# Optimization experiments

Measured on AMD Instinct MI355X. Metric: run time of the kernel, lower is better.

Reference implementation:

```python
import jax, jax.numpy as jnp
import numpy as np

B, CIN, COUT, KH, KW = 8, 64, 128, 3, 3
H = W = 64
STRIDE, PAD = 1, 1
G = 1  # deformable groups


def setup_inputs() -> dict:
    key = jax.random.key(0)
    k1, k2, k3 = jax.random.split(key, 3)
    rgb = jax.random.normal(k1, (B, CIN, H, W), dtype=jnp.float32)
    # torchvision layout: [B, 2*G*KH*KW, Ho, Wo], (dy, dx) pairs per kernel tap
    offsets = jax.random.normal(k2, (B, 2 * G * KH * KW, H, W), dtype=jnp.float32)
    # xavier_uniform for weight [COUT, CIN, KH, KW]
    fan_in, fan_out = CIN * KH * KW, COUT * KH * KW
    a = float(np.sqrt(6.0 / (fan_in + fan_out)))
    weight = jax.random.uniform(k3, (COUT, CIN, KH, KW), dtype=jnp.float32, minval=-a, maxval=a)
    bias = jnp.zeros((COUT,), dtype=jnp.float32)
    return {"rgb": rgb, "offsets": offsets, "weight": weight, "bias": bias}


def _deform_conv2d(rgb, offsets, weight, bias):
    b, cin, h, w = rgb.shape
    cout, _, kh, kw = weight.shape
    K = kh * kw
    ho = (h + 2 * PAD - kh) // STRIDE + 1
    wo = (w + 2 * PAD - kw) // STRIDE + 1
    cg = cin // G  # channels per deformable group

    off = offsets.reshape(b, G, K, 2, ho, wo)
    dy, dx = off[:, :, :, 0], off[:, :, :, 1]  # [b, G, K, ho, wo]

    ky, kx = jnp.meshgrid(jnp.arange(kh), jnp.arange(kw), indexing="ij")
    ky = ky.reshape(K).astype(jnp.float32)
    kx = kx.reshape(K).astype(jnp.float32)
    base_y = (jnp.arange(ho) * STRIDE - PAD).astype(jnp.float32)
    base_x = (jnp.arange(wo) * STRIDE - PAD).astype(jnp.float32)

    # sampling coordinates: p0 + kernel tap + learned offset -> [b, G, K, ho, wo]
    y = base_y[None, None, None, :, None] + ky[None, None, :, None, None] + dy
    x = base_x[None, None, None, None, :] + kx[None, None, :, None, None] + dx

    y0 = jnp.floor(y)
    x0 = jnp.floor(x)
    fy = y - y0
    fx = x - x0
    y0i = y0.astype(jnp.int32)
    x0i = x0.astype(jnp.int32)

    x_flat = rgb.reshape(b, G, cg, h * w)
    P = K * ho * wo

    def gather_corner(yc, xc, wgt):
        valid = (yc >= 0) & (yc < h) & (xc >= 0) & (xc < w)
        idx = jnp.clip(yc, 0, h - 1) * w + jnp.clip(xc, 0, w - 1)
        wgt = jnp.where(valid, wgt, 0.0).reshape(b, G, 1, P)
        vals = jnp.take_along_axis(x_flat, idx.reshape(b, G, 1, P), axis=3)
        return vals * wgt

    col = (
        gather_corner(y0i, x0i, (1 - fy) * (1 - fx))
        + gather_corner(y0i, x0i + 1, (1 - fy) * fx)
        + gather_corner(y0i + 1, x0i, fy * (1 - fx))
        + gather_corner(y0i + 1, x0i + 1, fy * fx)
    )  # [b, G, cg, K*ho*wo]

    col = col.reshape(b, cin * K, ho * wo)
    out = jnp.einsum("ok,bkp->bop", weight.reshape(cout, cin * K), col)
    return out.reshape(b, cout, ho, wo) + bias[None, :, None, None]


def reference(rgb, offsets, weight, bias):
    return _deform_conv2d(rgb, offsets, weight, bias)
```

## Files before the change

### kernel.cpp

```cpp
#include <hip/hip_runtime.h>

#define COUT_  128
#define KP     1024
#define CAPR   20
#define IMGC   (21 * 64)
#define IMGBUF (4 * IMGC)
#define COLU   36
#define COLBUF (64 * COLU)
#define WS_NEED (size_t)(COUT_ * KP * 2 + 8ull * 64 * 64 * 64 * 4)

#if __has_builtin(__builtin_amdgcn_fdot2_f32_bf16)
#define HAS_DOT2 1
#else
#define HAS_DOT2 0
#endif

typedef __attribute__((ext_vector_type(8))) __bf16 bf16x8;
typedef __attribute__((ext_vector_type(2))) __bf16 bf16x2;
typedef unsigned short u16x8 __attribute__((ext_vector_type(8)));
typedef __attribute__((ext_vector_type(4))) float f32x4;

__device__ __forceinline__ unsigned int f2bf(float f) {
    union { float f; unsigned int u; } c; c.f = f;
    unsigned int u = c.u;
    u += 0x7fffu + ((u >> 16) & 1u);
    return u >> 16;
}
__device__ __forceinline__ float bitsf(unsigned int u) {
    union { unsigned int u; float f; } c; c.u = u; return c.f;
}
__device__ __forceinline__ unsigned int pk2bf(float lo, float hi) {
    return f2bf(lo) | (f2bf(hi) << 16);
}
__device__ __forceinline__ bf16x2 mk_bf2(float lo, float hi) {
    unsigned int u = pk2bf(lo, hi);
    return __builtin_bit_cast(bf16x2, u);
}
__device__ __forceinline__ void gl_lds16(const unsigned int* g, unsigned int* l) {
    __builtin_amdgcn_global_load_lds(
        (const __attribute__((address_space(1))) unsigned int*)g,
        (__attribute__((address_space(3))) unsigned int*)l, 16, 0, 0);
}

__global__ void prep_weight(const float* __restrict__ w, unsigned short* __restrict__ wbf) {
    int idx = blockIdx.x * 256 + threadIdx.x;
    if (idx >= COUT_ * KP) return;
    int cout = idx >> 10, r = idx & 1023;
    int quad = r >> 6, j2 = r & 63;
    int k = j2 >> 2, j = j2 & 3;
    unsigned short v = 0;
    if (k < 9) {
        int cin = quad * 4 + j;
        v = (unsigned short)f2bf(w[(cout * 64 + cin) * 9 + k]);
    }
    wbf[idx] = v;
}

__global__ void prep_rgb(const float* __restrict__ rgb, unsigned int* __restrict__ rgbp) {
    int idx = blockIdx.x * 256 + threadIdx.x;
    float a = rgb[idx];
    float nb = ((idx & 63) == 63) ? 0.f : rgb[idx + 1];
    rgbp[idx] = f2bf(a) | (f2bf(nb) << 16);
}

template<bool PREP>
__launch_bounds__(256, 2)
__global__ void deform_mfma6(const float* __restrict__ rgb,
                             const unsigned int* __restrict__ rgbp,
                             const float* __restrict__ off,
                             const unsigned short* __restrict__ wbf,
                             const float* __restrict__ bias,
                             float* __restrict__ out) {
    __shared__ unsigned int S[2 * COLBUF + 2 * IMGBUF];
    __shared__ int sYmin, sYmax;
    unsigned int* imgU = S + 2 * COLBUF;

    const int t    = threadIdx.x;
    const int bid  = blockIdx.x;
    const int b    = bid & 7;
    const int ho   = bid >> 3;
    const int lane = t & 63;
    const int wv   = t >> 6;
    const int px   = lane;
    const int ln15 = lane & 15;
    const int q    = lane >> 4;

    const float* offb = off + b * (2 * 9 * 4096);

    {
        uint4* S4 = (uint4*)S;
        for (int i = t; i < (2 * COLBUF + 2 * IMGBUF) / 4; i += 256)
            S4[i] = make_uint4(0, 0, 0, 0);
    }
    if (t == 0) { sYmin = 64; sYmax = -1; }
    __syncthreads();

    float m_fy[3], m_fx[3]; int m_y0[3], m_x0[3];
    int lmin = 64, lmax = -1;
#pragma unroll
    for (int ti = 0; ti < 3; ti++) {
        const int kt = (ti < 2) ? (wv + ti * 4) : 8;
        const float dy = offb[((2 * kt)     * 64 + ho) * 64 + px];
        const float dx = offb[((2 * kt + 1) * 64 + ho) * 64 + px];
        const float y = (float)(ho - 1 + kt / 3) + dy;
        const float x = (float)(px - 1 + kt % 3) + dx;
        const float y0f = floorf(y), x0f = floorf(x);
        m_fy[ti] = y - y0f; m_fx[ti] = x - x0f;
        m_y0[ti] = (int)y0f; m_x0[ti] = (int)x0f;
        const int r0 = min(max(m_y0[ti], 0), 63), r1 = min(max(m_y0[ti] + 1, 0), 63);
        lmin = min(lmin, r0); lmax = max(lmax, r1);
    }
    atomicMin(&sYmin, lmin); atomicMax(&sYmax, lmax);
    __syncthreads();
    const int ymin  = sYmin;
    const int nrows = sYmax - ymin + 1;
    const int nr4   = min((nrows + 3) & ~3, CAPR);
    const int ymin2 = max(0, min(ymin, 64 - nr4));

    float4 sv[5];
    auto stage_dma = [&](int gg) {
        const unsigned int* gp = rgbp + ((unsigned)(b * 64 + gg * 4 + wv) * 64 + ymin2) * 64 + lane * 4;
        unsigned int* lp = imgU + (gg & 1) * IMGBUF + wv * IMGC;
        for (int r4 = 0; r4 < nr4; r4 += 4) gl_lds16(gp + r4 * 64, lp + r4 * 64);
    };
    auto stage_load = [&](int gg) {
        const float* gp = rgb + ((unsigned)(b * 64 + gg * 4 + wv) * 64 + ymin2 + (lane >> 4)) * 64 + (lane & 15) * 4;
        int n = 0;
        for (int r4 = 0; r4 < nr4; r4 += 4, n++) sv[n] = *(const float4*)(gp + r4 * 64);
    };
    auto stage_write = [&](int gg) {
        unsigned int* lp = imgU + (gg & 1) * IMGBUF + wv * IMGC + (lane >> 4) * 64 + (lane & 15) * 4;
        int n = 0;
        for (int r4 = 0; r4 < nr4; r4 += 4, n++) {
            const float4 v = sv[n];
            unsigned int b0 = f2bf(v.x), b1 = f2bf(v.y), b2 = f2bf(v.z), b3 = f2bf(v.w);
            unsigned int nb = __shfl(b0, lane + 1);
            if ((lane & 15) == 15) nb = 0;
            uint4 pk;
            pk.x = b0 | (b1 << 16); pk.y = b1 | (b2 << 16);
            pk.z = b2 | (b3 << 16); pk.w = b3 | (nb << 16);
            *(uint4*)(lp + r4 * 64) = pk;
        }
    };

    int ma[3];
#if HAS_DOT2
    bf16x2 wtp[3], wbp[3];
#else
    float mw[3][4];
#endif
#pragma unroll
    for (int ti = 0; ti < 3; ti++) {
        const int y0 = m_y0[ti], x0 = m_x0[ti];
        const float fy = m_fy[ti], fx = m_fx[ti];
        const int r0 = y0 - ymin2;
        const float wy0 = (y0 >= 0  && y0 < 64) ? (1.f - fy) : 0.f;
        const float wy1 = (y0 >= -1 && y0 < 63) ? fy         : 0.f;
        const bool ylo = (r0 < 0);
        const float wtop = ylo ? wy1 : wy0;
        const float wbot = ylo ? 0.f : wy1;
        const int r0c = ylo ? 0 : min(r0, nr4 - 1);
        const float wx0 = (x0 >= 0  && x0 < 64) ? (1.f - fx) : 0.f;
        const float wx1 = (x0 >= -1 && x0 < 63) ? fx         : 0.f;
        const bool xlo = (x0 < 0);
        const float wA = xlo ? wx1 : wx0;
        const float wB = xlo ? 0.f : wx1;
        const int xc = min(max(x0, 0), 63);
        ma[ti] = r0c * 64 + xc;
#if HAS_DOT2
        wtp[ti] = mk_bf2(wtop * wA, wtop * wB);
        wbp[ti] = mk_bf2(wbot * wA, wbot * wB);
#else
        mw[ti][0] = wtop * wA; mw[ti][1] = wtop * wB;
        mw[ti][2] = wbot * wA; mw[ti][3] = wbot * wB;
#endif
    }

    f32x4 acc[2][4] = {};
    const unsigned short* wrow0 = wbf + (wv * 32 + ln15) * KP;
    const unsigned short* wrow1 = wrow0 + 16 * KP;
    const unsigned short* col16 = (const unsigned short*)S;

    auto interp1 = [&](const unsigned int* pl, int ti) -> float {
        const unsigned int* p = pl + ma[ti];
        const unsigned int tp = p[0];
        const unsigned int bp = p[64];
#if HAS_DOT2
        float r = __builtin_amdgcn_fdot2_f32_bf16(__builtin_bit_cast(bf16x2, tp), wtp[ti], 0.f, false);
        return  __builtin_amdgcn_fdot2_f32_bf16(__builtin_bit_cast(bf16x2, bp), wbp[ti], r, false);
#else
        return mw[ti][0] * bitsf(tp << 16) + mw[ti][1] * bitsf(tp & 0xffff0000u)
             + mw[ti][2] * bitsf(bp << 16) + mw[ti][3] * bitsf(bp & 0xffff0000u);
#endif
    };
    auto gather = [&](int g) {
        const unsigned int* ib = imgU + (g & 1) * IMGBUF;
        unsigned int* cb = S + (g & 1) * COLBUF + px * COLU;
#pragma unroll
        for (int ti = 0; ti < 2; ti++) {
            const int kt = wv + ti * 4;
            uint2 w2;
            w2.x = pk2bf(interp1(ib, ti),            interp1(ib + IMGC, ti));
            w2.y = pk2bf(interp1(ib + 2 * IMGC, ti), interp1(ib + 3 * IMGC, ti));
            *(uint2*)&cb[kt * 2] = w2;
        }
        if (wv == (g & 3))
            cb[16] = pk2bf(interp1(ib, 2),            interp1(ib + IMGC, 2));
        if (wv == ((g + 2) & 3))
            cb[17] = pk2bf(interp1(ib + 2 * IMGC, 2), interp1(ib + 3 * IMGC, 2));
    };
    auto mfma_steps = [&](int gg) {
#pragma unroll
        for (int sg = 0; sg < 2; sg++) {
            const int s = 2 * gg + sg;
            const u16x8 a0u = *(const u16x8*)(wrow0 + s * 32 + q * 8);
            const u16x8 a1u = *(const u16x8*)(wrow1 + s * 32 + q * 8);
            const bf16x8 a0 = __builtin_bit_cast(bf16x8, a0u);
            const bf16x8 a1 = __builtin_bit_cast(bf16x8, a1u);
#pragma unroll
            for (int nj = 0; nj < 4; nj++) {
                const u16x8 bu = *(const u16x8*)(col16 + (gg & 1) * (COLBUF * 2)
                                                 + (nj * 16 + ln15) * (COLU * 2) + sg * 32 + q * 8);
                const bf16x8 bv = __builtin_bit_cast(bf16x8, bu);
                acc[0][nj] = __builtin_amdgcn_mfma_f32_16x16x32_bf16(a0, bv, acc[0][nj], 0, 0, 0);
                acc[1][nj] = __builtin_amdgcn_mfma_f32_16x16x32_bf16(a1, bv, acc[1][nj], 0, 0, 0);
            }
        }
    };

    if (PREP) stage_dma(0); else stage_load(0);
    if (!PREP) stage_write(0);
    __syncthreads();

    for (int g = 0; g < 16; g++) {
        if (g + 1 < 16) { if (PREP) stage_dma(g + 1); else stage_load(g + 1); }
        if (g > 0) mfma_steps(g - 1);
        gather(g);
        if (!PREP && g + 1 < 16) stage_write(g + 1);
        __syncthreads();
    }
    mfma_steps(15);

#pragma unroll
    for (int mi = 0; mi < 2; mi++) {
#pragma unroll
        for (int r = 0; r < 4; r++) {
            const int cout = wv * 32 + mi * 16 + q * 4 + r;
            const float bv = bias[cout];
            float* orow = out + ((b * COUT_ + cout) * 64 + ho) * 64;
#pragma unroll
            for (int nj = 0; nj < 4; nj++)
                orow[nj * 16 + ln15] = acc[mi][nj][r] + bv;
        }
    }
}

extern "C" void kernel_launch(void* const* d_in, const int* in_sizes, int n_in,
                              void* d_out, int out_size, void* d_ws, size_t ws_size,
                              hipStream_t stream) {
    const float* rgb  = (const float*)d_in[0];
    const float* off  = (const float*)d_in[1];
    const float* w    = (const float*)d_in[2];
    const float* bias = (const float*)d_in[3];
    float* out = (float*)d_out;
    unsigned short* wbf = (unsigned short*)d_ws;
    unsigned int* rgbp  = (unsigned int*)((char*)d_ws + COUT_ * KP * 2);

    prep_weight<<<(COUT_ * KP + 255) / 256, 256, 0, stream>>>(w, wbf);
    if (ws_size >= WS_NEED) {
        prep_rgb<<<8 * 64 * 4096 / 256, 256, 0, stream>>>(rgb, rgbp);
        deform_mfma6<true><<<512, 256, 0, stream>>>(rgb, rgbp, off, wbf, bias, out);
    } else {
        deform_mfma6<false><<<512, 256, 0, stream>>>(rgb, nullptr, off, wbf, bias, out);
    }
}
```

Baseline: 106.9 us.

## Fuse prep kernels, use wave-shuffle reduction, trim LDS zeroing, reorder gather/MFMA

Merges the weight and rgb preparation kernels into one launch to remove a kernel launch and its gap. Replaces the shared-memory atomic min/max row-range reduction with wave shuffles plus a small shared array. Zeroes only the LDS padding regions instead of the whole buffer, and moves the gather ahead of the MFMA step in the pipelined loop. It also switches the bf16 conversion to native casts, which risks different instruction selection and rounding behaviour.

```diff
diff --git a/kernel.cpp b/kernel.cpp
--- a/kernel.cpp
+++ b/kernel.cpp
@@ -30,11 +30,16 @@
     union { unsigned int u; float f; } c; c.u = u; return c.f;
 }
 __device__ __forceinline__ unsigned int pk2bf(float lo, float hi) {
-    return f2bf(lo) | (f2bf(hi) << 16);
+    bf16x2 v;
+    v[0] = (__bf16)lo;
+    v[1] = (__bf16)hi;
+    return __builtin_bit_cast(unsigned int, v);
 }
 __device__ __forceinline__ bf16x2 mk_bf2(float lo, float hi) {
-    unsigned int u = pk2bf(lo, hi);
-    return __builtin_bit_cast(bf16x2, u);
+    bf16x2 v;
+    v[0] = (__bf16)lo;
+    v[1] = (__bf16)hi;
+    return v;
 }
 __device__ __forceinline__ void gl_lds16(const unsigned int* g, unsigned int* l) {
     __builtin_amdgcn_global_load_lds(
@@ -42,25 +47,28 @@
         (__attribute__((address_space(3))) unsigned int*)l, 16, 0, 0);
 }
 
-__global__ void prep_weight(const float* __restrict__ w, unsigned short* __restrict__ wbf) {
-    int idx = blockIdx.x * 256 + threadIdx.x;
-    if (idx >= COUT_ * KP) return;
-    int cout = idx >> 10, r = idx & 1023;
-    int quad = r >> 6, j2 = r & 63;
-    int k = j2 >> 2, j = j2 & 3;
-    unsigned short v = 0;
-    if (k < 9) {
-        int cin = quad * 4 + j;
-        v = (unsigned short)f2bf(w[(cout * 64 + cin) * 9 + k]);
-    }
-    wbf[idx] = v;
-}
-
-__global__ void prep_rgb(const float* __restrict__ rgb, unsigned int* __restrict__ rgbp) {
-    int idx = blockIdx.x * 256 + threadIdx.x;
-    float a = rgb[idx];
-    float nb = ((idx & 63) == 63) ? 0.f : rgb[idx + 1];
-    rgbp[idx] = f2bf(a) | (f2bf(nb) << 16);
+__global__ void prep_all(const float* __restrict__ w, unsigned short* __restrict__ wbf,
+                         const float* __restrict__ rgb, unsigned int* __restrict__ rgbp,
+                         const int nrgb) {
+    const int blk = blockIdx.x;
+    if (blk < nrgb) {
+        const int idx = blk * 256 + threadIdx.x;
+        const float a = rgb[idx];
+        const float nb = ((idx & 63) == 63) ? 0.f : rgb[idx + 1];
+        rgbp[idx] = pk2bf(a, nb);
+    } else {
+        const int idx = (blk - nrgb) * 256 + threadIdx.x;
+        if (idx >= COUT_ * KP) return;
+        const int cout = idx >> 10, r = idx & 1023;
+        const int quad = r >> 6, j2 = r & 63;
+        const int k = j2 >> 2, j = j2 & 3;
+        unsigned short v = 0;
+        if (k < 9) {
+            const int cin = quad * 4 + j;
+            v = (unsigned short)f2bf(w[(cout * 64 + cin) * 9 + k]);
+        }
+        wbf[idx] = v;
+    }
 }
 
 template<bool PREP>
@@ -72,7 +80,7 @@
                              const float* __restrict__ bias,
                              float* __restrict__ out) {
     __shared__ unsigned int S[2 * COLBUF + 2 * IMGBUF];
-    __shared__ int sYmin, sYmax;
+    __shared__ int sW[8];
     unsigned int* imgU = S + 2 * COLBUF;
 
     const int t    = threadIdx.x;
@@ -86,14 +94,6 @@
     const int q    = lane >> 4;
 
     const float* offb = off + b * (2 * 9 * 4096);
-
-    {
-        uint4* S4 = (uint4*)S;
-        for (int i = t; i < (2 * COLBUF + 2 * IMGBUF) / 4; i += 256)
-            S4[i] = make_uint4(0, 0, 0, 0);
-    }
-    if (t == 0) { sYmin = 64; sYmax = -1; }
-    __syncthreads();
 
     float m_fy[3], m_fx[3]; int m_y0[3], m_x0[3];
     int lmin = 64, lmax = -1;
@@ -110,12 +110,30 @@
         const int r0 = min(max(m_y0[ti], 0), 63), r1 = min(max(m_y0[ti] + 1, 0), 63);
         lmin = min(lmin, r0); lmax = max(lmax, r1);
     }
-    atomicMin(&sYmin, lmin); atomicMax(&sYmax, lmax);
+#pragma unroll
+    for (int d = 1; d < 64; d <<= 1) {
+        lmin = min(lmin, __shfl_xor(lmin, d));
+        lmax = max(lmax, __shfl_xor(lmax, d));
+    }
+    if (lane == 0) { sW[wv] = lmin; sW[4 + wv] = lmax; }
     __syncthreads();
-    const int ymin  = sYmin;
-    const int nrows = sYmax - ymin + 1;
+    const int ymin  = min(min(sW[0], sW[1]), min(sW[2], sW[3]));
+    const int ymax  = max(max(sW[4], sW[5]), max(sW[6], sW[7]));
+    const int nrows = ymax - ymin + 1;
     const int nr4   = min((nrows + 3) & ~3, CAPR);
     const int ymin2 = max(0, min(ymin, 64 - nr4));
+
+    {
+        const uint4 z4 = make_uint4(0, 0, 0, 0);
+        for (int i = t; i < 512; i += 256) {
+            const int buf = i >> 8, j = i & 255, p_ = j >> 2, r = j & 3;
+            *(uint4*)&S[buf * COLBUF + p_ * COLU + 16 + r * 4] = z4;
+        }
+        if (t < 128) {
+            const int buf = t >> 6, pl = (t >> 4) & 3, c4 = t & 15;
+            *(uint4*)&imgU[buf * IMGBUF + pl * IMGC + nr4 * 64 + c4 * 4] = z4;
+        }
+    }
 
     float4 sv[5];
     auto stage_dma = [&](int gg) {
@@ -125,21 +143,23 @@
     };
     auto stage_load = [&](int gg) {
         const float* gp = rgb + ((unsigned)(b * 64 + gg * 4 + wv) * 64 + ymin2 + (lane >> 4)) * 64 + (lane & 15) * 4;
-        int n = 0;
-        for (int r4 = 0; r4 < nr4; r4 += 4, n++) sv[n] = *(const float4*)(gp + r4 * 64);
+#pragma unroll
+        for (int n = 0; n < 5; n++)
+            if (n * 4 < nr4) sv[n] = *(const float4*)(gp + n * 4 * 64);
     };
     auto stage_write = [&](int gg) {
         unsigned int* lp = imgU + (gg & 1) * IMGBUF + wv * IMGC + (lane >> 4) * 64 + (lane & 15) * 4;
-        int n = 0;
-        for (int r4 = 0; r4 < nr4; r4 += 4, n++) {
-            const float4 v = sv[n];
-            unsigned int b0 = f2bf(v.x), b1 = f2bf(v.y), b2 = f2bf(v.z), b3 = f2bf(v.w);
-            unsigned int nb = __shfl(b0, lane + 1);
-            if ((lane & 15) == 15) nb = 0;
-            uint4 pk;
-            pk.x = b0 | (b1 << 16); pk.y = b1 | (b2 << 16);
-            pk.z = b2 | (b3 << 16); pk.w = b3 | (nb << 16);
-            *(uint4*)(lp + r4 * 64) = pk;
+#pragma unroll
+        for (int n = 0; n < 5; n++) {
+            if (n * 4 < nr4) {
+                const float4 v = sv[n];
+                float nf = __shfl(v.x, lane + 1);
+                if ((lane & 15) == 15) nf = 0.f;
+                uint4 pk;
+                pk.x = pk2bf(v.x, v.y); pk.y = pk2bf(v.y, v.z);
+                pk.z = pk2bf(v.z, v.w); pk.w = pk2bf(v.w, nf);
+                *(uint4*)(lp + n * 4 * 64) = pk;
+            }
         }
     };
 
@@ -228,14 +248,13 @@
         }
     };
 
-    if (PREP) stage_dma(0); else stage_load(0);
-    if (!PREP) stage_write(0);
+    if (PREP) stage_dma(0); else { stage_load(0); stage_write(0); }
     __syncthreads();
 
     for (int g = 0; g < 16; g++) {
         if (g + 1 < 16) { if (PREP) stage_dma(g + 1); else stage_load(g + 1); }
+        gather(g);
         if (g > 0) mfma_steps(g - 1);
-        gather(g);
         if (!PREP && g + 1 < 16) stage_write(g + 1);
         __syncthreads();
     }
@@ -266,11 +285,11 @@
     unsigned short* wbf = (unsigned short*)d_ws;
     unsigned int* rgbp  = (unsigned int*)((char*)d_ws + COUT_ * KP * 2);
 
-    prep_weight<<<(COUT_ * KP + 255) / 256, 256, 0, stream>>>(w, wbf);
     if (ws_size >= WS_NEED) {
-        prep_rgb<<<8 * 64 * 4096 / 256, 256, 0, stream>>>(rgb, rgbp);
+        prep_all<<<8192 + 512, 256, 0, stream>>>(w, wbf, rgb, rgbp, 8192);
         deform_mfma6<true><<<512, 256, 0, stream>>>(rgb, rgbp, off, wbf, bias, out);
     } else {
+        prep_all<<<512, 256, 0, stream>>>(w, wbf, rgb, nullptr, 0);
         deform_mfma6<false><<<512, 256, 0, stream>>>(rgb, nullptr, off, wbf, bias, out);
     }
 }
```

Result: faster. 103.3 us (-3.4%).
